# Kernel optimization log

Measured on AMD Instinct MI355X. Metric: run time of the kernel, lower is better.

The kernel has to match this reference:

```python
import jax, jax.numpy as jnp
import numpy as np

N, D_OUT, D_LAT, D_Z = 65536, 128, 64, 64


def setup_inputs() -> dict:
    key = jax.random.key(0)
    ks = jax.random.split(key, 6)
    return {
        "target": jax.random.normal(ks[0], (N, D_OUT), dtype=jnp.float32),
        "output": jax.random.normal(ks[1], (N, D_OUT), dtype=jnp.float32),
        "mean": jax.random.normal(ks[2], (N, D_LAT), dtype=jnp.float32),
        "log_variance": jax.random.normal(ks[3], (N, D_LAT), dtype=jnp.float32),
        "z_t": jax.random.normal(ks[4], (N, D_Z), dtype=jnp.float32),
        "z_t_tau": jax.random.normal(ks[5], (N, D_Z), dtype=jnp.float32),
    }


def reference(target, output, mean, log_variance, z_t, z_t_tau):
    # ELBO: KL(q||N(0,1)) per-sample summed over latent dim, then batch mean
    kl = -0.5 * jnp.sum(log_variance - jnp.exp(log_variance) - mean ** 2 + 1.0, axis=1)
    kl = jnp.mean(kl)
    # reconstruction MSE (weights=None path)
    reconstruction = jnp.mean((output - target) ** 2)
    elbo_loss = reconstruction + kl

    # autocorrelation: diagonal of z_t_centered @ z_t_tau_centered.T is just
    # a rowwise dot product -> O(N*D) instead of O(N^2*D)
    z_t_centered = z_t - jnp.mean(z_t, axis=0)          # [N, D_z]
    z_t_tau_centered = z_t_tau - jnp.mean(z_t_tau, axis=0)
    diag = jnp.sum(z_t_centered * z_t_tau_centered, axis=1)  # [N]
    auto_correlation_loss = -jnp.mean(diag)

    # torch .std() is unbiased (ddof=1)
    std_t = jnp.std(z_t, axis=0, ddof=1)                # [D_z]
    std_tau = jnp.std(z_t_tau, axis=0, ddof=1)
    auto_correlation_loss = auto_correlation_loss / jnp.dot(std_t, std_tau)

    return elbo_loss + auto_correlation_loss
```

## Files before the change

### kernel.cpp

```cpp
#include <hip/hip_runtime.h>

constexpr int N_ROWS  = 65536;
constexpr int BLOCKS  = 2048;
constexpr int THREADS = 256;
constexpr int T_TOT   = BLOCKS * THREADS;

constexpr int R_IT = (N_ROWS * 128 / 4) / T_TOT;
constexpr int K_IT = (N_ROWS *  64 / 4) / T_TOT;
constexpr int Z_IT = K_IT;

constexpr int NVAL = 324;
constexpr int NREP = 64;


__global__ __launch_bounds__(THREADS) void vde_main(
    const float4* __restrict__ target,
    const float4* __restrict__ output,
    const float4* __restrict__ mean,
    const float4* __restrict__ logvar,
    const float4* __restrict__ zt,
    const float4* __restrict__ ztau,
    float* __restrict__ ws)
{
    const int tid  = blockIdx.x * THREADS + threadIdx.x;
    const int lane = threadIdx.x & 63;
    const int wave = threadIdx.x >> 6;
    float* rep = ws + (blockIdx.x & (NREP - 1)) * NVAL;

    float4 ro[R_IT], rt[R_IT];
    #pragma unroll
    for (int it = 0; it < R_IT; ++it) {
        ro[it] = output[tid + it * T_TOT];
        rt[it] = target[tid + it * T_TOT];
    }
    float4 klv[K_IT], km[K_IT];
    #pragma unroll
    for (int it = 0; it < K_IT; ++it) {
        klv[it] = logvar[tid + it * T_TOT];
        km[it]  = mean[tid + it * T_TOT];
    }
    float4 za[Z_IT], zb[Z_IT];
    #pragma unroll
    for (int it = 0; it < Z_IT; ++it) {
        za[it] = zt[tid + it * T_TOT];
        zb[it] = ztau[tid + it * T_TOT];
    }

    float recon = 0.f;
    #pragma unroll
    for (int it = 0; it < R_IT; ++it) {
        float dx = ro[it].x - rt[it].x, dy = ro[it].y - rt[it].y;
        float dz = ro[it].z - rt[it].z, dw = ro[it].w - rt[it].w;
        recon += dx * dx + dy * dy + dz * dz + dw * dw;
    }

    float kls = 0.f;
    #pragma unroll
    for (int it = 0; it < K_IT; ++it) {
        float4 lv = klv[it], m = km[it];
        kls += (lv.x - __expf(lv.x) - m.x * m.x + 1.f)
             + (lv.y - __expf(lv.y) - m.y * m.y + 1.f)
             + (lv.z - __expf(lv.z) - m.z * m.z + 1.f)
             + (lv.w - __expf(lv.w) - m.w * m.w + 1.f);
    }

    float s_t[4] = {0,0,0,0}, s_t2[4] = {0,0,0,0};
    float s_a[4] = {0,0,0,0}, s_a2[4] = {0,0,0,0}, s_c[4] = {0,0,0,0};
    #pragma unroll
    for (int it = 0; it < Z_IT; ++it) {
        const float ax[4] = {za[it].x, za[it].y, za[it].z, za[it].w};
        const float bx[4] = {zb[it].x, zb[it].y, zb[it].z, zb[it].w};
        #pragma unroll
        for (int e = 0; e < 4; ++e) {
            s_t[e]  += ax[e];        s_a[e]  += bx[e];
            s_t2[e] += ax[e]*ax[e];  s_a2[e] += bx[e]*bx[e];
            s_c[e]  += ax[e]*bx[e];
        }
    }

    #pragma unroll
    for (int m = 32; m >= 1; m >>= 1) {
        recon += __shfl_xor(recon, m);
        kls   += __shfl_xor(kls, m);
    }
    __shared__ float ssc[4][2];
    if (lane == 0) { ssc[wave][0] = recon; ssc[wave][1] = kls; }

    float vals[20];
    #pragma unroll
    for (int e = 0; e < 4; ++e) {
        vals[e*5+0] = s_t[e];  vals[e*5+1] = s_a[e];
        vals[e*5+2] = s_t2[e]; vals[e*5+3] = s_a2[e];
        vals[e*5+4] = s_c[e];
    }
    #pragma unroll
    for (int v = 0; v < 20; ++v) {
        vals[v] += __shfl_xor(vals[v], 16);
        vals[v] += __shfl_xor(vals[v], 32);
    }
    __shared__ float sred[4][16][20];
    if (lane < 16) {
        #pragma unroll
        for (int v = 0; v < 20; ++v) sred[wave][lane][v] = vals[v];
    }
    __syncthreads();

    if (threadIdx.x == 0) {
        atomicAdd(&rep[0], ssc[0][0] + ssc[1][0] + ssc[2][0] + ssc[3][0]);
        atomicAdd(&rep[1], ssc[0][1] + ssc[1][1] + ssc[2][1] + ssc[3][1]);
    }
    for (int i = threadIdx.x; i < 320; i += THREADS) {
        const int g = i / 20, v = i % 20;
        const float s = sred[0][g][v] + sred[1][g][v] + sred[2][g][v] + sred[3][g][v];
        const int e = v / 5, st = v % 5;
        atomicAdd(&rep[2 + st * 64 + (g * 4 + e)], s);
    }
}

__global__ __launch_bounds__(256) void vde_collapse(
    const float* __restrict__ ws, float* __restrict__ sums)
{
    const int lane = threadIdx.x & 63;
    const int j = blockIdx.x * 4 + (threadIdx.x >> 6);
    float v = ws[lane * NVAL + j];
    #pragma unroll
    for (int m = 32; m >= 1; m >>= 1) v += __shfl_xor(v, m);
    if (lane == 0) sums[j] = v;
}

__global__ __launch_bounds__(64) void vde_finalize(
    const float* __restrict__ sums, float* __restrict__ out)
{
    const int j = threadIdx.x;
    const float Nf = (float)N_ROWS;

    const float sum_t  = sums[2 + 0*64 + j];
    const float sum_a  = sums[2 + 1*64 + j];
    const float sum_t2 = sums[2 + 2*64 + j];
    const float sum_a2 = sums[2 + 3*64 + j];
    const float sum_c  = sums[2 + 4*64 + j];

    const float mu_t = sum_t / Nf, mu_a = sum_a / Nf;
    float diag = sum_c - Nf * mu_t * mu_a;
    const float var_t = (sum_t2 - Nf * mu_t * mu_t) / (Nf - 1.f);
    const float var_a = (sum_a2 - Nf * mu_a * mu_a) / (Nf - 1.f);
    float sp = sqrtf(var_t) * sqrtf(var_a);

    #pragma unroll
    for (int m = 32; m >= 1; m >>= 1) {
        diag += __shfl_xor(diag, m);
        sp   += __shfl_xor(sp, m);
    }
    if (j == 0) {
        const float recon_f = sums[0] / (Nf * 128.f);
        const float kl_f    = -0.5f * sums[1] / Nf;
        out[0] = recon_f + kl_f - (diag / Nf) / sp;
    }
}

extern "C" void kernel_launch(void* const* d_in, const int* in_sizes, int n_in,
                              void* d_out, int out_size, void* d_ws, size_t ws_size,
                              hipStream_t stream) {
    const float4* target = (const float4*)d_in[0];
    const float4* output = (const float4*)d_in[1];
    const float4* mean   = (const float4*)d_in[2];
    const float4* logvar = (const float4*)d_in[3];
    const float4* zt     = (const float4*)d_in[4];
    const float4* ztau   = (const float4*)d_in[5];
    float* ws  = (float*)d_ws;
    float* out = (float*)d_out;

    hipMemsetAsync(ws, 0, NREP * NVAL * sizeof(float), stream);
    vde_main<<<BLOCKS, THREADS, 0, stream>>>(target, output, mean, logvar, zt, ztau, ws);
    vde_collapse<<<81, 256, 0, stream>>>(ws, ws + NREP * NVAL);
    vde_finalize<<<1, 64, 0, stream>>>(ws + NREP * NVAL, out);
}
```

Measured before the change: 160.5 us.

## Specialize blocks per loss term and merge collapse/finalize into one tail kernel

```diff
diff --git a/kernel.cpp b/kernel.cpp
--- a/kernel.cpp
+++ b/kernel.cpp
@@ -1,13 +1,11 @@
 #include <hip/hip_runtime.h>
 
 constexpr int N_ROWS  = 65536;
-constexpr int BLOCKS  = 2048;
 constexpr int THREADS = 256;
-constexpr int T_TOT   = BLOCKS * THREADS;
-
-constexpr int R_IT = (N_ROWS * 128 / 4) / T_TOT;
-constexpr int K_IT = (N_ROWS *  64 / 4) / T_TOT;
-constexpr int Z_IT = K_IT;
+constexpr int B_MSE = 1024, B_KL = 512, B_Z = 512;
+constexpr int BLOCKS = B_MSE + B_KL + B_Z;
+constexpr int F4_BLK = 2048;
+constexpr int IT     = F4_BLK / THREADS;
 
 constexpr int NVAL = 324;
 constexpr int NREP = 64;
@@ -22,139 +20,131 @@
     const float4* __restrict__ ztau,
     float* __restrict__ ws)
 {
-    const int tid  = blockIdx.x * THREADS + threadIdx.x;
     const int lane = threadIdx.x & 63;
     const int wave = threadIdx.x >> 6;
     float* rep = ws + (blockIdx.x & (NREP - 1)) * NVAL;
 
-    float4 ro[R_IT], rt[R_IT];
-    #pragma unroll
-    for (int it = 0; it < R_IT; ++it) {
-        ro[it] = output[tid + it * T_TOT];
-        rt[it] = target[tid + it * T_TOT];
-    }
-    float4 klv[K_IT], km[K_IT];
-    #pragma unroll
-    for (int it = 0; it < K_IT; ++it) {
-        klv[it] = logvar[tid + it * T_TOT];
-        km[it]  = mean[tid + it * T_TOT];
-    }
-    float4 za[Z_IT], zb[Z_IT];
-    #pragma unroll
-    for (int it = 0; it < Z_IT; ++it) {
-        za[it] = zt[tid + it * T_TOT];
-        zb[it] = ztau[tid + it * T_TOT];
-    }
+    __shared__ float ssc[4];
+    __shared__ float sred[4][16][20];
 
-    float recon = 0.f;
-    #pragma unroll
-    for (int it = 0; it < R_IT; ++it) {
-        float dx = ro[it].x - rt[it].x, dy = ro[it].y - rt[it].y;
-        float dz = ro[it].z - rt[it].z, dw = ro[it].w - rt[it].w;
-        recon += dx * dx + dy * dy + dz * dz + dw * dw;
-    }
+    if (blockIdx.x < B_MSE) {
+        const int base = blockIdx.x * F4_BLK + threadIdx.x;
+        float recon = 0.f;
+        #pragma unroll
+        for (int it = 0; it < IT; ++it) {
+            float4 o = output[base + it * THREADS];
+            float4 t = target[base + it * THREADS];
+            float dx = o.x - t.x, dy = o.y - t.y;
+            float dz = o.z - t.z, dw = o.w - t.w;
+            recon += dx * dx + dy * dy + dz * dz + dw * dw;
+        }
+        #pragma unroll
+        for (int m = 32; m >= 1; m >>= 1) recon += __shfl_xor(recon, m);
+        if (lane == 0) ssc[wave] = recon;
+        __syncthreads();
+        if (threadIdx.x == 0)
+            atomicAdd(&rep[0], ssc[0] + ssc[1] + ssc[2] + ssc[3]);
 
-    float kls = 0.f;
-    #pragma unroll
-    for (int it = 0; it < K_IT; ++it) {
-        float4 lv = klv[it], m = km[it];
-        kls += (lv.x - __expf(lv.x) - m.x * m.x + 1.f)
-             + (lv.y - __expf(lv.y) - m.y * m.y + 1.f)
-             + (lv.z - __expf(lv.z) - m.z * m.z + 1.f)
-             + (lv.w - __expf(lv.w) - m.w * m.w + 1.f);
-    }
+    } else if (blockIdx.x < B_MSE + B_KL) {
+        const int base = (blockIdx.x - B_MSE) * F4_BLK + threadIdx.x;
+        float kls = 0.f;
+        #pragma unroll
+        for (int it = 0; it < IT; ++it) {
+            float4 lv = logvar[base + it * THREADS];
+            float4 m  = mean[base + it * THREADS];
+            kls += (lv.x - __expf(lv.x) - m.x * m.x + 1.f)
+                 + (lv.y - __expf(lv.y) - m.y * m.y + 1.f)
+                 + (lv.z - __expf(lv.z) - m.z * m.z + 1.f)
+                 + (lv.w - __expf(lv.w) - m.w * m.w + 1.f);
+        }
+        #pragma unroll
+        for (int m = 32; m >= 1; m >>= 1) kls += __shfl_xor(kls, m);
+        if (lane == 0) ssc[wave] = kls;
+        __syncthreads();
+        if (threadIdx.x == 0)
+            atomicAdd(&rep[1], ssc[0] + ssc[1] + ssc[2] + ssc[3]);
 
-    float s_t[4] = {0,0,0,0}, s_t2[4] = {0,0,0,0};
-    float s_a[4] = {0,0,0,0}, s_a2[4] = {0,0,0,0}, s_c[4] = {0,0,0,0};
-    #pragma unroll
-    for (int it = 0; it < Z_IT; ++it) {
-        const float ax[4] = {za[it].x, za[it].y, za[it].z, za[it].w};
-        const float bx[4] = {zb[it].x, zb[it].y, zb[it].z, zb[it].w};
+    } else {
+        const int base = (blockIdx.x - B_MSE - B_KL) * F4_BLK + threadIdx.x;
+        float s_t[4] = {0,0,0,0}, s_t2[4] = {0,0,0,0};
+        float s_a[4] = {0,0,0,0}, s_a2[4] = {0,0,0,0}, s_c[4] = {0,0,0,0};
+        #pragma unroll
+        for (int it = 0; it < IT; ++it) {
+            float4 a = zt[base + it * THREADS];
+            float4 b = ztau[base + it * THREADS];
+            const float ax[4] = {a.x, a.y, a.z, a.w};
+            const float bx[4] = {b.x, b.y, b.z, b.w};
+            #pragma unroll
+            for (int e = 0; e < 4; ++e) {
+                s_t[e]  += ax[e];        s_a[e]  += bx[e];
+                s_t2[e] += ax[e]*ax[e];  s_a2[e] += bx[e]*bx[e];
+                s_c[e]  += ax[e]*bx[e];
+            }
+        }
+        float vals[20];
         #pragma unroll
         for (int e = 0; e < 4; ++e) {
-            s_t[e]  += ax[e];        s_a[e]  += bx[e];
-            s_t2[e] += ax[e]*ax[e];  s_a2[e] += bx[e]*bx[e];
-            s_c[e]  += ax[e]*bx[e];
+            vals[e*5+0] = s_t[e];  vals[e*5+1] = s_a[e];
+            vals[e*5+2] = s_t2[e]; vals[e*5+3] = s_a2[e];
+            vals[e*5+4] = s_c[e];
+        }
+        #pragma unroll
+        for (int v = 0; v < 20; ++v) {
+            vals[v] += __shfl_xor(vals[v], 16);
+            vals[v] += __shfl_xor(vals[v], 32);
+        }
+        if (lane < 16) {
+            #pragma unroll
+            for (int v = 0; v < 20; ++v) sred[wave][lane][v] = vals[v];
+        }
+        __syncthreads();
+        for (int i = threadIdx.x; i < 320; i += THREADS) {
+            const int g = i / 20, v = i % 20;
+            const float s = sred[0][g][v] + sred[1][g][v]
+                          + sred[2][g][v] + sred[3][g][v];
+            const int e = v / 5, st = v % 5;
+            atomicAdd(&rep[2 + st * 64 + (g * 4 + e)], s);
         }
     }
+}
 
-    #pragma unroll
-    for (int m = 32; m >= 1; m >>= 1) {
-        recon += __shfl_xor(recon, m);
-        kls   += __shfl_xor(kls, m);
-    }
-    __shared__ float ssc[4][2];
-    if (lane == 0) { ssc[wave][0] = recon; ssc[wave][1] = kls; }
-
-    float vals[20];
-    #pragma unroll
-    for (int e = 0; e < 4; ++e) {
-        vals[e*5+0] = s_t[e];  vals[e*5+1] = s_a[e];
-        vals[e*5+2] = s_t2[e]; vals[e*5+3] = s_a2[e];
-        vals[e*5+4] = s_c[e];
-    }
-    #pragma unroll
-    for (int v = 0; v < 20; ++v) {
-        vals[v] += __shfl_xor(vals[v], 16);
-        vals[v] += __shfl_xor(vals[v], 32);
-    }
-    __shared__ float sred[4][16][20];
-    if (lane < 16) {
+__global__ __launch_bounds__(256) void vde_tail(
+    const float* __restrict__ ws, float* __restrict__ out)
+{
+    __shared__ float sums[NVAL];
+    for (int j = threadIdx.x; j < NVAL; j += 256) {
+        float s = 0.f;
         #pragma unroll
-        for (int v = 0; v < 20; ++v) sred[wave][lane][v] = vals[v];
+        for (int r = 0; r < NREP; ++r) s += ws[r * NVAL + j];
+        sums[j] = s;
     }
     __syncthreads();
 
-    if (threadIdx.x == 0) {
-        atomicAdd(&rep[0], ssc[0][0] + ssc[1][0] + ssc[2][0] + ssc[3][0]);
-        atomicAdd(&rep[1], ssc[0][1] + ssc[1][1] + ssc[2][1] + ssc[3][1]);
-    }
-    for (int i = threadIdx.x; i < 320; i += THREADS) {
-        const int g = i / 20, v = i % 20;
-        const float s = sred[0][g][v] + sred[1][g][v] + sred[2][g][v] + sred[3][g][v];
-        const int e = v / 5, st = v % 5;
-        atomicAdd(&rep[2 + st * 64 + (g * 4 + e)], s);
-    }
-}
+    if (threadIdx.x < 64) {
+        const int j = threadIdx.x;
+        const float Nf = (float)N_ROWS;
+        const float sum_t  = sums[2 + 0*64 + j];
+        const float sum_a  = sums[2 + 1*64 + j];
+        const float sum_t2 = sums[2 + 2*64 + j];
+        const float sum_a2 = sums[2 + 3*64 + j];
+        const float sum_c  = sums[2 + 4*64 + j];
 
-__global__ __launch_bounds__(256) void vde_collapse(
-    const float* __restrict__ ws, float* __restrict__ sums)
-{
-    const int lane = threadIdx.x & 63;
-    const int j = blockIdx.x * 4 + (threadIdx.x >> 6);
-    float v = ws[lane * NVAL + j];
-    #pragma unroll
-    for (int m = 32; m >= 1; m >>= 1) v += __shfl_xor(v, m);
-    if (lane == 0) sums[j] = v;
-}
+        const float mu_t = sum_t / Nf, mu_a = sum_a / Nf;
+        float diag = sum_c - Nf * mu_t * mu_a;
+        const float var_t = (sum_t2 - Nf * mu_t * mu_t) / (Nf - 1.f);
+        const float var_a = (sum_a2 - Nf * mu_a * mu_a) / (Nf - 1.f);
+        float sp = sqrtf(var_t) * sqrtf(var_a);
 
-__global__ __launch_bounds__(64) void vde_finalize(
-    const float* __restrict__ sums, float* __restrict__ out)
-{
-    const int j = threadIdx.x;
-    const float Nf = (float)N_ROWS;
-
-    const float sum_t  = sums[2 + 0*64 + j];
-    const float sum_a  = sums[2 + 1*64 + j];
-    const float sum_t2 = sums[2 + 2*64 + j];
-    const float sum_a2 = sums[2 + 3*64 + j];
-    const float sum_c  = sums[2 + 4*64 + j];
-
-    const float mu_t = sum_t / Nf, mu_a = sum_a / Nf;
-    float diag = sum_c - Nf * mu_t * mu_a;
-    const float var_t = (sum_t2 - Nf * mu_t * mu_t) / (Nf - 1.f);
-    const float var_a = (sum_a2 - Nf * mu_a * mu_a) / (Nf - 1.f);
-    float sp = sqrtf(var_t) * sqrtf(var_a);
-
-    #pragma unroll
-    for (int m = 32; m >= 1; m >>= 1) {
-        diag += __shfl_xor(diag, m);
-        sp   += __shfl_xor(sp, m);
-    }
-    if (j == 0) {
-        const float recon_f = sums[0] / (Nf * 128.f);
-        const float kl_f    = -0.5f * sums[1] / Nf;
-        out[0] = recon_f + kl_f - (diag / Nf) / sp;
+        #pragma unroll
+        for (int m = 32; m >= 1; m >>= 1) {
+            diag += __shfl_xor(diag, m);
+            sp   += __shfl_xor(sp, m);
+        }
+        if (j == 0) {
+            const float recon_f = sums[0] / (Nf * 128.f);
+            const float kl_f    = -0.5f * sums[1] / Nf;
+            out[0] = recon_f + kl_f - (diag / Nf) / sp;
+        }
     }
 }
 
@@ -172,6 +162,5 @@
 
     hipMemsetAsync(ws, 0, NREP * NVAL * sizeof(float), stream);
     vde_main<<<BLOCKS, THREADS, 0, stream>>>(target, output, mean, logvar, zt, ztau, ws);
-    vde_collapse<<<81, 256, 0, stream>>>(ws, ws + NREP * NVAL);
-    vde_finalize<<<1, 64, 0, stream>>>(ws + NREP * NVAL, out);
+    vde_tail<<<1, 256, 0, stream>>>(ws, out);
 }
```

Measured after the change: 158.4 us. Within noise of the previous version (-1.3%).
